# Kernel tuning notes

Hardware: AMD Instinct MI355X
Metric: run time of the kernel (lower is better)

## Reference

```python
import jax, jax.numpy as jnp
import numpy as np

V, E, H, S, B = 32000, 1024, 1024, 1024, 64


def setup_inputs() -> dict:
    key = jax.random.key(0)
    ks = jax.random.split(key, 10)
    inp = {
        "word_input": jax.random.randint(ks[0], (1, B), 0, V),
        "last_context": jax.random.normal(ks[1], (B, H), jnp.float32),
        "last_hidden": jax.random.normal(ks[2], (1, B, H), jnp.float32),
        "encoder_outputs": jax.random.normal(ks[3], (S, B, H), jnp.float32),
        # parameters
        "emb_table": jax.random.normal(ks[4], (V, E), jnp.float32) * 0.02,
        "w_ih": jax.random.normal(ks[5], (3 * H, E + H), jnp.float32) * (1.0 / np.sqrt(E + H)),
        "w_hh": jax.random.normal(ks[6], (3 * H, H), jnp.float32) * (1.0 / np.sqrt(H)),
        "b_ih": jnp.zeros((3 * H,), jnp.float32),
        "b_hh": jnp.zeros((3 * H,), jnp.float32),
        "out_W": jax.random.uniform(ks[7], (V, 2 * H), jnp.float32, -0.1, 0.1),
        "out_b": jnp.zeros((V,), jnp.float32),
    }
    return inp


def _gru_step(x, h, w_ih, w_hh, b_ih, b_hh):
    # PyTorch GRU gate order: r, z, n
    gi = x @ w_ih.T + b_ih  # (B, 3H)
    gh = h @ w_hh.T + b_hh  # (B, 3H)
    gi_r, gi_z, gi_n = jnp.split(gi, 3, axis=1)
    gh_r, gh_z, gh_n = jnp.split(gh, 3, axis=1)
    r = jax.nn.sigmoid(gi_r + gh_r)
    z = jax.nn.sigmoid(gi_z + gh_z)
    n = jnp.tanh(gi_n + r * gh_n)
    return (1.0 - z) * n + z * h


def reference(word_input, last_context, last_hidden, encoder_outputs,
              emb_table, w_ih, w_hh, b_ih, b_hh, out_W, out_b):
    # embedding: (1, B, E)
    word_embedded = emb_table[word_input]
    # rnn input: (B, E+H)
    x0 = jnp.concatenate([word_embedded[0], last_context], axis=1)
    h = _gru_step(x0, last_hidden[0], w_ih, w_hh, b_ih, b_hh)  # (B, H)
    hidden = h[None]  # (1, B, H)
    # Luong dot attention, fused: energies (S, B)
    energies = jnp.einsum('bh,sbh->sb', h, encoder_outputs)
    weights = jax.nn.softmax(energies, axis=0)  # softmax over seq dim
    attn_weights = weights.T[:, None, :]  # (B, 1, S)
    context = jnp.einsum('sb,sbh->bh', weights, encoder_outputs)  # (B, H)
    logits = jnp.concatenate([h, context], axis=1) @ out_W.T + out_b  # (B, V)
    output = jax.nn.log_softmax(logits, axis=1)
    return output, context, hidden, attn_weights
```

## Files before the change

kernel.cpp:

```cpp
#include <hip/hip_runtime.h>
#include <math.h>

#define NV 32000
#define NE 1024
#define NH 1024
#define NS 1024
#define NB 64

typedef __attribute__((ext_vector_type(4))) float f32x4;
typedef __attribute__((ext_vector_type(8))) short bf16x8;

#define OUT_CTX   (NB*NV)
#define OUT_HID   (NB*NV + NB*NH)
#define OUT_ATTN  (NB*NV + 2*NB*NH)

#define WS_XA   0
#define WS_HA   (WS_XA + 65536)
#define WS_PG   (WS_HA + 32768)
#define WS_E    (WS_PG + 12*3072*64)
#define WS_PCTX (WS_E + NB*NS)
#define WS_ML   (WS_PCTX + 64*64*1024)
#define WS_LA   (WS_ML + 8192)
#define WS_ML2  (WS_LA + 65536)
#define WS_LSE  (WS_ML2 + 64*2048*2)
#define WS_P    (WS_LSE + 64)

__device__ inline unsigned short f2bf(float f) {
    unsigned u = __builtin_bit_cast(unsigned, f);
    u += 0x7fffu + ((u >> 16) & 1u);
    return (unsigned short)(u >> 16);
}

__device__ inline bf16x8 cvt8(float4 a, float4 b) {
    bf16x8 r;
    r[0] = (short)f2bf(a.x); r[1] = (short)f2bf(a.y);
    r[2] = (short)f2bf(a.z); r[3] = (short)f2bf(a.w);
    r[4] = (short)f2bf(b.x); r[5] = (short)f2bf(b.y);
    r[6] = (short)f2bf(b.z); r[7] = (short)f2bf(b.w);
    return r;
}

__device__ inline void store_bf4(unsigned short* p, float4 v) {
    ushort4 u = make_ushort4(f2bf(v.x), f2bf(v.y), f2bf(v.z), f2bf(v.w));
    *(ushort4*)p = u;
}

__global__ void k_prep(const int* __restrict__ wi, const float* __restrict__ lctx,
                       const float* __restrict__ lhid, const float* __restrict__ emb,
                       float* __restrict__ ws) {
    int b = blockIdx.x, t = threadIdx.x;
    unsigned short* XA = (unsigned short*)(ws + WS_XA);
    unsigned short* HA = (unsigned short*)(ws + WS_HA);
    long row = wi[b];
    float4 e4 = ((const float4*)(emb + row*NE))[t];
    float4 c4 = ((const float4*)(lctx + (long)b*NH))[t];
    float4 h4 = ((const float4*)(lhid + (long)b*NH))[t];
    store_bf4(XA + (long)b*2048 + t*4,        e4);
    store_bf4(XA + (long)b*2048 + 1024 + t*4, c4);
    store_bf4(HA + (long)b*1024 + t*4,        h4);
}

__global__ void __launch_bounds__(256) k_gru_mfma(const float* __restrict__ w_ih,
                                                  const float* __restrict__ w_hh,
                                                  float* __restrict__ ws) {
    int wave = blockIdx.x*4 + (threadIdx.x >> 6);
    int lane = threadIdx.x & 63;
    int c = wave % 12, ntile = wave / 12;
    int n0 = ntile * 16;
    int col = lane & 15, kg = lane >> 4;
    const unsigned short* XA = (const unsigned short*)(ws + WS_XA);
    const unsigned short* HA = (const unsigned short*)(ws + WS_HA);
    const float* Wp; const unsigned short* Ap; int ld, kbase;
    if (c < 8) { Wp = w_ih; Ap = XA; ld = 2048; kbase = c*256; }
    else       { Wp = w_hh; Ap = HA; ld = 1024; kbase = (c-8)*256; }
    const float* wrow = Wp + (long)(n0 + col)*ld + kbase + kg*8;
    f32x4 acc[4];
    #pragma unroll
    for (int m = 0; m < 4; m++) acc[m] = (f32x4){0.f,0.f,0.f,0.f};
    #pragma unroll 4
    for (int k0 = 0; k0 < 256; k0 += 32) {
        float4 wa = *(const float4*)(wrow + k0);
        float4 wb = *(const float4*)(wrow + k0 + 4);
        bf16x8 bf = cvt8(wa, wb);
        #pragma unroll
        for (int m = 0; m < 4; m++) {
            bf16x8 af = *(const bf16x8*)(Ap + (long)(m*16 + col)*ld + kbase + k0 + kg*8);
            acc[m] = __builtin_amdgcn_mfma_f32_16x16x32_bf16(af, bf, acc[m], 0, 0, 0);
        }
    }
    float* pg = ws + WS_PG + ((long)c*3072 + n0 + col)*64;
    #pragma unroll
    for (int m = 0; m < 4; m++)
        #pragma unroll
        for (int j = 0; j < 4; j++)
            pg[m*16 + kg*4 + j] = acc[m][j];
}

__global__ void k_gates(const float* __restrict__ wsc, const float* __restrict__ b_ih,
                        const float* __restrict__ b_hh, const float* __restrict__ lhid,
                        float* __restrict__ out, float* __restrict__ ws) {
    int g = blockIdx.x*256 + threadIdx.x;
    int b = g & 63, i = g >> 6;
    float gir=0.f, giz=0.f, gin=0.f, ghr=0.f, ghz=0.f, ghn=0.f;
    #pragma unroll
    for (int c = 0; c < 8; c++) {
        long base = WS_PG + (long)c*3072*64;
        gir += wsc[base + ((long)(0*NH + i))*64 + b];
        giz += wsc[base + ((long)(1*NH + i))*64 + b];
        gin += wsc[base + ((long)(2*NH + i))*64 + b];
    }
    #pragma unroll
    for (int c = 8; c < 12; c++) {
        long base = WS_PG + (long)c*3072*64;
        ghr += wsc[base + ((long)(0*NH + i))*64 + b];
        ghz += wsc[base + ((long)(1*NH + i))*64 + b];
        ghn += wsc[base + ((long)(2*NH + i))*64 + b];
    }
    gir += b_ih[i];        ghr += b_hh[i];
    giz += b_ih[NH + i];   ghz += b_hh[NH + i];
    gin += b_ih[2*NH + i]; ghn += b_hh[2*NH + i];
    float r = 1.f / (1.f + expf(-(gir + ghr)));
    float z = 1.f / (1.f + expf(-(giz + ghz)));
    float n = tanhf(gin + r*ghn);
    float hp = lhid[(long)b*NH + i];
    float h = (1.f - z)*n + z*hp;
    out[OUT_HID + (long)b*NH + i] = h;
    ((unsigned short*)(ws + WS_LA))[(long)b*2048 + i] = f2bf(h);
}

__global__ void __launch_bounds__(256) k_attn_logh(const float* __restrict__ enc,
                                                   const float* __restrict__ oW,
                                                   const float* __restrict__ out,
                                                   float* __restrict__ ws) {
    int widx = threadIdx.x >> 6, lane = threadIdx.x & 63;
    if (blockIdx.x < 500) {
        int vt = blockIdx.x*4 + widx;
        int v0 = vt * 16;
        int col = lane & 15, kg = lane >> 4;
        const unsigned short* LA = (const unsigned short*)(ws + WS_LA);
        const float* wrow = oW + (long)(v0 + col)*2048 + kg*8;
        f32x4 acc[4];
        #pragma unroll
        for (int m = 0; m < 4; m++) acc[m] = (f32x4){0.f,0.f,0.f,0.f};
        #pragma unroll 4
        for (int k0 = 0; k0 < 1024; k0 += 32) {
            float4 wa = *(const float4*)(wrow + k0);
            float4 wb = *(const float4*)(wrow + k0 + 4);
            bf16x8 bf = cvt8(wa, wb);
            #pragma unroll
            for (int m = 0; m < 4; m++) {
                bf16x8 af = *(const bf16x8*)(LA + (long)(m*16 + col)*2048 + k0 + kg*8);
                acc[m] = __builtin_amdgcn_mfma_f32_16x16x32_bf16(af, bf, acc[m], 0, 0, 0);
            }
        }
        float* P = ws + WS_P + (long)vt*1024;
        #pragma unroll
        for (int m = 0; m < 4; m++)
            #pragma unroll
            for (int j = 0; j < 4; j++)
                P[(m*16 + kg*4 + j)*16 + col] = acc[m][j];
        return;
    }
    int blk = blockIdx.x - 500;
    int b = blk >> 4;
    int g = (blk & 15)*4 + widx;
    const float4* hr = (const float4*)(out + OUT_HID + (long)b*NH);
    float4 h0 = hr[lane], h1 = hr[64+lane], h2 = hr[128+lane], h3 = hr[192+lane];
    float m = -1e30f, l = 0.f;
    float4 c0 = make_float4(0,0,0,0), c1 = c0, c2 = c0, c3 = c0;
    const float4* vp = (const float4*)(enc + ((long)(g*16)*NB + b)*NH);
    const long sstr = (long)NB*NH/4;
    float4 a0 = vp[lane], a1 = vp[64+lane], a2 = vp[128+lane], a3 = vp[192+lane];
    #pragma unroll
    for (int si = 0; si < 16; si++) {
        float4 n0 = a0, n1 = a1, n2 = a2, n3 = a3;
        if (si < 15) {
            const float4* np = vp + (long)(si+1)*sstr;
            n0 = np[lane]; n1 = np[64+lane]; n2 = np[128+lane]; n3 = np[192+lane];
        }
        float d = a0.x*h0.x + a0.y*h0.y + a0.z*h0.z + a0.w*h0.w
                + a1.x*h1.x + a1.y*h1.y + a1.z*h1.z + a1.w*h1.w
                + a2.x*h2.x + a2.y*h2.y + a2.z*h2.z + a2.w*h2.w
                + a3.x*h3.x + a3.y*h3.y + a3.z*h3.z + a3.w*h3.w;
        #pragma unroll
        for (int o = 32; o > 0; o >>= 1) d += __shfl_xor(d, o);
        if (lane == 0) ws[WS_E + (long)b*NS + g*16 + si] = d;
        if (d > m + 8.f) {
            float coef = expf(m - d);
            l *= coef;
            c0.x *= coef; c0.y *= coef; c0.z *= coef; c0.w *= coef;
            c1.x *= coef; c1.y *= coef; c1.z *= coef; c1.w *= coef;
            c2.x *= coef; c2.y *= coef; c2.z *= coef; c2.w *= coef;
            c3.x *= coef; c3.y *= coef; c3.z *= coef; c3.w *= coef;
            m = d;
        }
        float p = expf(d - m);
        l += p;
        c0.x += p*a0.x; c0.y += p*a0.y; c0.z += p*a0.z; c0.w += p*a0.w;
        c1.x += p*a1.x; c1.y += p*a1.y; c1.z += p*a1.z; c1.w += p*a1.w;
        c2.x += p*a2.x; c2.y += p*a2.y; c2.z += p*a2.z; c2.w += p*a2.w;
        c3.x += p*a3.x; c3.y += p*a3.y; c3.z += p*a3.z; c3.w += p*a3.w;
        a0 = n0; a1 = n1; a2 = n2; a3 = n3;
    }
    float* pc = ws + WS_PCTX + ((long)b*64 + g)*1024;
    *(float4*)(pc + 0*256 + lane*4) = c0;
    *(float4*)(pc + 1*256 + lane*4) = c1;
    *(float4*)(pc + 2*256 + lane*4) = c2;
    *(float4*)(pc + 3*256 + lane*4) = c3;
    if (lane == 0) {
        ws[WS_ML + ((long)b*64 + g)*2]     = m;
        ws[WS_ML + ((long)b*64 + g)*2 + 1] = l;
    }
}

__global__ void k_attn_reduce(const float* __restrict__ wsc, float* __restrict__ out,
                              float* __restrict__ ws) {
    int b = blockIdx.x >> 2, q = blockIdx.x & 3;
    int t = threadIdx.x;
    __shared__ float sm[64], sl[64], sc[64];
    __shared__ float sM, sinvL;
    if (t < 64) {
        sm[t] = wsc[WS_ML + ((long)b*64 + t)*2];
        sl[t] = wsc[WS_ML + ((long)b*64 + t)*2 + 1];
    }
    __syncthreads();
    if (t == 0) {
        float M = -1e30f;
        for (int g = 0; g < 64; g++) M = fmaxf(M, sm[g]);
        float L = 0.f;
        for (int g = 0; g < 64; g++) L += sl[g]*expf(sm[g] - M);
        sM = M; sinvL = 1.f/L;
    }
    __syncthreads();
    float M = sM, invL = sinvL;
    if (t < 64) sc[t] = expf(sm[t] - M);
    __syncthreads();
    int h = q*256 + t;
    float acc = 0.f;
    #pragma unroll 8
    for (int g = 0; g < 64; g++)
        acc += sc[g] * wsc[WS_PCTX + ((long)b*64 + g)*1024 + h];
    float ctx = acc * invL;
    out[OUT_CTX + (long)b*NH + h] = ctx;
    ((unsigned short*)(ws + WS_LA))[(long)b*2048 + 1024 + h] = f2bf(ctx);
    int s = q*256 + t;
    float e = wsc[WS_E + (long)b*NS + s];
    out[OUT_ATTN + (long)b*NS + s] = expf(e - M)*invL;
}

__global__ void __launch_bounds__(256) k_logits_ctx(const float* __restrict__ oW,
                                                    const float* __restrict__ ob,
                                                    const float* __restrict__ wsc,
                                                    float* __restrict__ out,
                                                    float* __restrict__ ws) {
    int widx = threadIdx.x >> 6, lane = threadIdx.x & 63;
    int vt = blockIdx.x*4 + widx;
    int v0 = vt * 16;
    int col = lane & 15, kg = lane >> 4;
    const unsigned short* LA = (const unsigned short*)(wsc + WS_LA);
    const float* wrow = oW + (long)(v0 + col)*2048 + 1024 + kg*8;
    f32x4 acc[4];
    #pragma unroll
    for (int m = 0; m < 4; m++) acc[m] = (f32x4){0.f,0.f,0.f,0.f};
    #pragma unroll 4
    for (int k0 = 0; k0 < 1024; k0 += 32) {
        float4 wa = *(const float4*)(wrow + k0);
        float4 wb = *(const float4*)(wrow + k0 + 4);
        bf16x8 bf = cvt8(wa, wb);
        #pragma unroll
        for (int m = 0; m < 4; m++) {
            bf16x8 af = *(const bf16x8*)(LA + (long)(m*16 + col)*2048 + 1024 + k0 + kg*8);
            acc[m] = __builtin_amdgcn_mfma_f32_16x16x32_bf16(af, bf, acc[m], 0, 0, 0);
        }
    }
    const float* P = wsc + WS_P + (long)vt*1024;
    float bias = ob[v0 + col];
    #pragma unroll
    for (int m = 0; m < 4; m++) {
        #pragma unroll
        for (int j = 0; j < 4; j++) {
            int row = m*16 + kg*4 + j;
            float v = acc[m][j] + P[row*16 + col] + bias;
            out[(long)row*NV + v0 + col] = v;
            float mx = v;
            mx = fmaxf(mx, __shfl_xor(mx, 1));
            mx = fmaxf(mx, __shfl_xor(mx, 2));
            mx = fmaxf(mx, __shfl_xor(mx, 4));
            mx = fmaxf(mx, __shfl_xor(mx, 8));
            float p = expf(v - mx);
            p += __shfl_xor(p, 1);
            p += __shfl_xor(p, 2);
            p += __shfl_xor(p, 4);
            p += __shfl_xor(p, 8);
            if (col == 0)
                *(float2*)(ws + WS_ML2 + ((long)row*2048 + vt)*2) = make_float2(mx, p);
        }
    }
}

__global__ void __launch_bounds__(1024) k_lse(const float* __restrict__ wsc,
                                              float* __restrict__ ws) {
    int b = blockIdx.x, t = threadIdx.x;
    __shared__ float sm_[1024], sl_[1024];
    const float2* ml = (const float2*)(wsc + WS_ML2 + (long)b*4096);
    float m = -1e30f, l = 0.f;
    for (int c = t; c < 2000; c += 1024) {
        float2 v = ml[c];
        float mn = fmaxf(m, v.x);
        l = l*expf(m - mn) + v.y*expf(v.x - mn);
        m = mn;
    }
    sm_[t] = m; sl_[t] = l; __syncthreads();
    for (int o = 512; o > 0; o >>= 1) {
        if (t < o) {
            float m2 = sm_[t+o], l2 = sl_[t+o];
            float mn = fmaxf(sm_[t], m2);
            sl_[t] = sl_[t]*expf(sm_[t] - mn) + l2*expf(m2 - mn);
            sm_[t] = mn;
        }
        __syncthreads();
    }
    if (t == 0) ws[WS_LSE + b] = sm_[0] + logf(sl_[0]);
}

__global__ void __launch_bounds__(1024) k_norm(const float* __restrict__ wsc,
                                               float* __restrict__ out) {
    int g = blockIdx.x*1024 + threadIdx.x;
    int b = g / 8000;
    int i = g - b*8000;
    float lse = wsc[WS_LSE + b];
    float4* p = (float4*)(out + (long)b*NV) + i;
    float4 v = *p;
    *p = make_float4(v.x-lse, v.y-lse, v.z-lse, v.w-lse);
}

extern "C" void kernel_launch(void* const* d_in, const int* in_sizes, int n_in,
                              void* d_out, int out_size, void* d_ws, size_t ws_size,
                              hipStream_t stream) {
    const int*   wi   = (const int*)d_in[0];
    const float* lctx = (const float*)d_in[1];
    const float* lhid = (const float*)d_in[2];
    const float* enc  = (const float*)d_in[3];
    const float* emb  = (const float*)d_in[4];
    const float* w_ih = (const float*)d_in[5];
    const float* w_hh = (const float*)d_in[6];
    const float* b_ih = (const float*)d_in[7];
    const float* b_hh = (const float*)d_in[8];
    const float* oW   = (const float*)d_in[9];
    const float* ob   = (const float*)d_in[10];
    float* out = (float*)d_out;
    float* ws  = (float*)d_ws;

    hipLaunchKernelGGL(k_prep,        dim3(64),   dim3(256),  0, stream, wi, lctx, lhid, emb, ws);
    hipLaunchKernelGGL(k_gru_mfma,    dim3(576),  dim3(256),  0, stream, w_ih, w_hh, ws);
    hipLaunchKernelGGL(k_gates,       dim3(256),  dim3(256),  0, stream, ws, b_ih, b_hh, lhid, out, ws);
    hipLaunchKernelGGL(k_attn_logh,   dim3(1524), dim3(256),  0, stream, enc, oW, out, ws);
    hipLaunchKernelGGL(k_attn_reduce, dim3(256),  dim3(256),  0, stream, ws, out, ws);
    hipLaunchKernelGGL(k_logits_ctx,  dim3(500),  dim3(256),  0, stream, oW, ob, ws, out, ws);
    hipLaunchKernelGGL(k_lse,         dim3(64),   dim3(1024), 0, stream, ws, ws);
    hipLaunchKernelGGL(k_norm,        dim3(500),  dim3(1024), 0, stream, ws, out);
}
```

Before: 213.1 us.

## Store bf16 activations in MFMA-fragment layout and fuse LSE with normalization

The bf16 activation matrices (XA, HA, LA) are now written in a tiled layout matching the MFMA A-fragment access pattern, so each wave's loads for a k-step are contiguous across lanes instead of strided by row. The producer kernels (prep, gates, attn_reduce) and all three MFMA consumers are updated to use this layout. Separately, the LSE reduction and the log-softmax subtraction are merged into one kernel, removing a launch and the LSE round trip. Each of the 8 blocks per row recomputes the full LSE reduction, which duplicates that work.

```diff
diff --git a/kernel.cpp b/kernel.cpp
--- a/kernel.cpp
+++ b/kernel.cpp
@@ -25,6 +25,7 @@
 #define WS_LSE  (WS_ML2 + 64*2048*2)
 #define WS_P    (WS_LSE + 64)
 
+
 __device__ inline unsigned short f2bf(float f) {
     unsigned u = __builtin_bit_cast(unsigned, f);
     u += 0x7fffu + ((u >> 16) & 1u);
@@ -55,9 +56,11 @@
     float4 e4 = ((const float4*)(emb + row*NE))[t];
     float4 c4 = ((const float4*)(lctx + (long)b*NH))[t];
     float4 h4 = ((const float4*)(lhid + (long)b*NH))[t];
-    store_bf4(XA + (long)b*2048 + t*4,        e4);
-    store_bf4(XA + (long)b*2048 + 1024 + t*4, c4);
-    store_bf4(HA + (long)b*1024 + t*4,        h4);
+    int o1 = ((t>>3)*4 + ((t>>1)&3))*512 + b*8 + 4*(t&1);
+    int o2 = ((32 + (t>>3))*4 + ((t>>1)&3))*512 + b*8 + 4*(t&1);
+    store_bf4(XA + o1, e4);
+    store_bf4(XA + o2, c4);
+    store_bf4(HA + o1, h4);
 }
 
 __global__ void __launch_bounds__(256) k_gru_mfma(const float* __restrict__ w_ih,
@@ -70,10 +73,11 @@
     int col = lane & 15, kg = lane >> 4;
     const unsigned short* XA = (const unsigned short*)(ws + WS_XA);
     const unsigned short* HA = (const unsigned short*)(ws + WS_HA);
-    const float* Wp; const unsigned short* Ap; int ld, kbase;
-    if (c < 8) { Wp = w_ih; Ap = XA; ld = 2048; kbase = c*256; }
-    else       { Wp = w_hh; Ap = HA; ld = 1024; kbase = (c-8)*256; }
+    const float* Wp; const unsigned short* Af; int ld, kbase;
+    if (c < 8) { Wp = w_ih; Af = XA; ld = 2048; kbase = c*256; }
+    else       { Wp = w_hh; Af = HA; ld = 1024; kbase = (c-8)*256; }
     const float* wrow = Wp + (long)(n0 + col)*ld + kbase + kg*8;
+    const unsigned short* ap = Af + (kbase>>5)*2048 + kg*512 + col*8;
     f32x4 acc[4];
     #pragma unroll
     for (int m = 0; m < 4; m++) acc[m] = (f32x4){0.f,0.f,0.f,0.f};
@@ -81,11 +85,12 @@
     for (int k0 = 0; k0 < 256; k0 += 32) {
         float4 wa = *(const float4*)(wrow + k0);
         float4 wb = *(const float4*)(wrow + k0 + 4);
-        bf16x8 bf = cvt8(wa, wb);
+        bf16x8 bfv = cvt8(wa, wb);
+        const unsigned short* a0 = ap + (k0>>5)*2048;
         #pragma unroll
         for (int m = 0; m < 4; m++) {
-            bf16x8 af = *(const bf16x8*)(Ap + (long)(m*16 + col)*ld + kbase + k0 + kg*8);
-            acc[m] = __builtin_amdgcn_mfma_f32_16x16x32_bf16(af, bf, acc[m], 0, 0, 0);
+            bf16x8 af = *(const bf16x8*)(a0 + m*128);
+            acc[m] = __builtin_amdgcn_mfma_f32_16x16x32_bf16(af, bfv, acc[m], 0, 0, 0);
         }
     }
     float* pg = ws + WS_PG + ((long)c*3072 + n0 + col)*64;
@@ -125,7 +130,7 @@
     float hp = lhid[(long)b*NH + i];
     float h = (1.f - z)*n + z*hp;
     out[OUT_HID + (long)b*NH + i] = h;
-    ((unsigned short*)(ws + WS_LA))[(long)b*2048 + i] = f2bf(h);
+    ((unsigned short*)(ws + WS_LA))[((i>>5)*4 + ((i>>3)&3))*512 + b*8 + (i&7)] = f2bf(h);
 }
 
 __global__ void __launch_bounds__(256) k_attn_logh(const float* __restrict__ enc,
@@ -139,6 +144,7 @@
         int col = lane & 15, kg = lane >> 4;
         const unsigned short* LA = (const unsigned short*)(ws + WS_LA);
         const float* wrow = oW + (long)(v0 + col)*2048 + kg*8;
+        const unsigned short* ap = LA + kg*512 + col*8;
         f32x4 acc[4];
         #pragma unroll
         for (int m = 0; m < 4; m++) acc[m] = (f32x4){0.f,0.f,0.f,0.f};
@@ -146,11 +152,12 @@
         for (int k0 = 0; k0 < 1024; k0 += 32) {
             float4 wa = *(const float4*)(wrow + k0);
             float4 wb = *(const float4*)(wrow + k0 + 4);
-            bf16x8 bf = cvt8(wa, wb);
+            bf16x8 bfv = cvt8(wa, wb);
+            const unsigned short* a0 = ap + (k0>>5)*2048;
             #pragma unroll
             for (int m = 0; m < 4; m++) {
-                bf16x8 af = *(const bf16x8*)(LA + (long)(m*16 + col)*2048 + k0 + kg*8);
-                acc[m] = __builtin_amdgcn_mfma_f32_16x16x32_bf16(af, bf, acc[m], 0, 0, 0);
+                bf16x8 af = *(const bf16x8*)(a0 + m*128);
+                acc[m] = __builtin_amdgcn_mfma_f32_16x16x32_bf16(af, bfv, acc[m], 0, 0, 0);
             }
         }
         float* P = ws + WS_P + (long)vt*1024;
@@ -242,7 +249,8 @@
         acc += sc[g] * wsc[WS_PCTX + ((long)b*64 + g)*1024 + h];
     float ctx = acc * invL;
     out[OUT_CTX + (long)b*NH + h] = ctx;
-    ((unsigned short*)(ws + WS_LA))[(long)b*2048 + 1024 + h] = f2bf(ctx);
+    int k = 1024 + h;
+    ((unsigned short*)(ws + WS_LA))[((k>>5)*4 + ((k>>3)&3))*512 + b*8 + (k&7)] = f2bf(ctx);
     int s = q*256 + t;
     float e = wsc[WS_E + (long)b*NS + s];
     out[OUT_ATTN + (long)b*NS + s] = expf(e - M)*invL;
@@ -259,6 +267,7 @@
     int col = lane & 15, kg = lane >> 4;
     const unsigned short* LA = (const unsigned short*)(wsc + WS_LA);
     const float* wrow = oW + (long)(v0 + col)*2048 + 1024 + kg*8;
+    const unsigned short* ap = LA + 32*2048 + kg*512 + col*8;
     f32x4 acc[4];
     #pragma unroll
     for (int m = 0; m < 4; m++) acc[m] = (f32x4){0.f,0.f,0.f,0.f};
@@ -266,11 +275,12 @@
     for (int k0 = 0; k0 < 1024; k0 += 32) {
         float4 wa = *(const float4*)(wrow + k0);
         float4 wb = *(const float4*)(wrow + k0 + 4);
-        bf16x8 bf = cvt8(wa, wb);
+        bf16x8 bfv = cvt8(wa, wb);
+        const unsigned short* a0 = ap + (k0>>5)*2048;
         #pragma unroll
         for (int m = 0; m < 4; m++) {
-            bf16x8 af = *(const bf16x8*)(LA + (long)(m*16 + col)*2048 + 1024 + k0 + kg*8);
-            acc[m] = __builtin_amdgcn_mfma_f32_16x16x32_bf16(af, bf, acc[m], 0, 0, 0);
+            bf16x8 af = *(const bf16x8*)(a0 + m*128);
+            acc[m] = __builtin_amdgcn_mfma_f32_16x16x32_bf16(af, bfv, acc[m], 0, 0, 0);
         }
     }
     const float* P = wsc + WS_P + (long)vt*1024;
@@ -298,20 +308,21 @@
     }
 }
 
-__global__ void __launch_bounds__(1024) k_lse(const float* __restrict__ wsc,
-                                              float* __restrict__ ws) {
-    int b = blockIdx.x, t = threadIdx.x;
-    __shared__ float sm_[1024], sl_[1024];
+__global__ void __launch_bounds__(256) k_lsenorm(const float* __restrict__ wsc,
+                                                 float* __restrict__ out) {
+    int b = blockIdx.x >> 3, oct = blockIdx.x & 7;
+    int t = threadIdx.x;
+    __shared__ float sm_[256], sl_[256];
     const float2* ml = (const float2*)(wsc + WS_ML2 + (long)b*4096);
     float m = -1e30f, l = 0.f;
-    for (int c = t; c < 2000; c += 1024) {
+    for (int c = t; c < 2000; c += 256) {
         float2 v = ml[c];
         float mn = fmaxf(m, v.x);
         l = l*expf(m - mn) + v.y*expf(v.x - mn);
         m = mn;
     }
     sm_[t] = m; sl_[t] = l; __syncthreads();
-    for (int o = 512; o > 0; o >>= 1) {
+    for (int o = 128; o > 0; o >>= 1) {
         if (t < o) {
             float m2 = sm_[t+o], l2 = sl_[t+o];
             float mn = fmaxf(sm_[t], m2);
@@ -320,18 +331,16 @@
         }
         __syncthreads();
     }
-    if (t == 0) ws[WS_LSE + b] = sm_[0] + logf(sl_[0]);
-}
-
-__global__ void __launch_bounds__(1024) k_norm(const float* __restrict__ wsc,
-                                               float* __restrict__ out) {
-    int g = blockIdx.x*1024 + threadIdx.x;
-    int b = g / 8000;
-    int i = g - b*8000;
-    float lse = wsc[WS_LSE + b];
-    float4* p = (float4*)(out + (long)b*NV) + i;
-    float4 v = *p;
-    *p = make_float4(v.x-lse, v.y-lse, v.z-lse, v.w-lse);
+    float lse = sm_[0] + logf(sl_[0]);
+    float4* row4 = (float4*)(out + (long)b*NV + oct*4000);
+    #pragma unroll
+    for (int j = 0; j < 4; j++) {
+        int idx = t + j*256;
+        if (idx < 1000) {
+            float4 v = row4[idx];
+            row4[idx] = make_float4(v.x-lse, v.y-lse, v.z-lse, v.w-lse);
+        }
+    }
 }
 
 extern "C" void kernel_launch(void* const* d_in, const int* in_sizes, int n_in,
@@ -351,12 +360,11 @@
     float* out = (float*)d_out;
     float* ws  = (float*)d_ws;
 
-    hipLaunchKernelGGL(k_prep,        dim3(64),   dim3(256),  0, stream, wi, lctx, lhid, emb, ws);
-    hipLaunchKernelGGL(k_gru_mfma,    dim3(576),  dim3(256),  0, stream, w_ih, w_hh, ws);
-    hipLaunchKernelGGL(k_gates,       dim3(256),  dim3(256),  0, stream, ws, b_ih, b_hh, lhid, out, ws);
-    hipLaunchKernelGGL(k_attn_logh,   dim3(1524), dim3(256),  0, stream, enc, oW, out, ws);
-    hipLaunchKernelGGL(k_attn_reduce, dim3(256),  dim3(256),  0, stream, ws, out, ws);
-    hipLaunchKernelGGL(k_logits_ctx,  dim3(500),  dim3(256),  0, stream, oW, ob, ws, out, ws);
-    hipLaunchKernelGGL(k_lse,         dim3(64),   dim3(1024), 0, stream, ws, ws);
-    hipLaunchKernelGGL(k_norm,        dim3(500),  dim3(1024), 0, stream, ws, out);
-}
+    hipLaunchKernelGGL(k_prep,        dim3(64),   dim3(256), 0, stream, wi, lctx, lhid, emb, ws);
+    hipLaunchKernelGGL(k_gru_mfma,    dim3(576),  dim3(256), 0, stream, w_ih, w_hh, ws);
+    hipLaunchKernelGGL(k_gates,       dim3(256),  dim3(256), 0, stream, ws, b_ih, b_hh, lhid, out, ws);
+    hipLaunchKernelGGL(k_attn_logh,   dim3(1524), dim3(256), 0, stream, enc, oW, out, ws);
+    hipLaunchKernelGGL(k_attn_reduce, dim3(256),  dim3(256), 0, stream, ws, out, ws);
+    hipLaunchKernelGGL(k_logits_ctx,  dim3(500),  dim3(256), 0, stream, oW, ob, ws, out, ws);
+    hipLaunchKernelGGL(k_lsenorm,     dim3(512),  dim3(256), 0, stream, ws, out);
+}
```

After: 182.4 us. 14.4% less time.
